# Kernel tuning notes

Hardware: AMD Instinct MI355X
Metric: run time of the kernel (lower is better)

Reference implementation:

```python
import jax, jax.numpy as jnp
import numpy as np

MARGIN = 0.2
W_HARD = 1.0
W_SOFT = 0.0
NORMALIZE = True
PD_EPS = 1e-6  # torch F.pairwise_distance eps used inside TripletMarginLoss


def setup_inputs() -> dict:
    key = jax.random.key(0)
    k1, k2, k3 = jax.random.split(key, 3)
    N, D = 8192, 128
    z = jax.random.normal(k1, (N, D), dtype=jnp.float32)
    labels = jax.random.randint(k2, (N,), 0, 16, dtype=jnp.int32)
    subjects = jax.random.randint(k3, (N,), 0, 32, dtype=jnp.int32)
    return {"z": z, "labels": labels, "subjects": subjects}


def _batch_hard(z, pos_mask, neg_mask, margin):
    # pairwise euclidean distances (cdist p=2); mining indices are ints, so
    # stop_gradient keeps vjp clean (matches torch: argmax/argmin detach).
    sq = jnp.sum(z * z, axis=1)
    d2 = sq[:, None] + sq[None, :] - 2.0 * (z @ z.T)
    dist = jax.lax.stop_gradient(jnp.sqrt(jnp.maximum(d2, 0.0)))
    inf = jnp.asarray(jnp.inf, dist.dtype)
    p_idx = jnp.argmax(jnp.where(pos_mask, dist, -inf), axis=1)  # hardest positive
    n_idx = jnp.argmin(jnp.where(neg_mask, dist, inf), axis=1)   # hardest negative
    valid = jnp.any(pos_mask, axis=1) & jnp.any(neg_mask, axis=1)
    a, p, n = z, z[p_idx], z[n_idx]
    d_ap = jnp.sqrt(jnp.sum((a - p + PD_EPS) ** 2, axis=1))
    d_an = jnp.sqrt(jnp.sum((a - n + PD_EPS) ** 2, axis=1))
    per = jnp.maximum(d_ap - d_an + margin, 0.0)
    cnt = jnp.sum(valid)
    loss = jnp.sum(per * valid) / jnp.maximum(cnt, 1).astype(per.dtype)
    return jnp.where(cnt > 0, loss, 0.0)


def reference(z, labels, subjects):
    if NORMALIZE:
        z = z / jnp.maximum(jnp.linalg.norm(z, axis=1, keepdims=True), 1e-12)
    N = z.shape[0]
    same_class = labels[:, None] == labels[None, :]
    same_subj = subjects[:, None] == subjects[None, :]
    not_eye = ~jnp.eye(N, dtype=bool)
    loss = 0.0
    denom = 0.0
    if W_HARD != 0:
        pos_hard = same_class & ~same_subj & not_eye
        neg_hard = ~same_class & same_subj & not_eye
        loss = loss + W_HARD * _batch_hard(z, pos_hard, neg_hard, MARGIN)
        denom += abs(W_HARD)
    if W_SOFT != 0:
        pos_soft = same_class & same_subj & not_eye
        neg_soft = ~same_class & ~same_subj & not_eye
        loss = loss + W_SOFT * _batch_hard(z, pos_soft, neg_soft, MARGIN)
        denom += abs(W_SOFT)
    return loss / max(denom, 1e-12)
```

## Files before the change

kernel.cpp:

```cpp
#include <hip/hip_runtime.h>
#include <math.h>

#define N 8192
#define D 128
#define MARGIN 0.2f
#define PD_EPS 1e-6f
#define NCHUNK 16
#define CHUNKJ (N / NCHUNK)

typedef __attribute__((ext_vector_type(8))) short bf16x8;
typedef __attribute__((ext_vector_type(4))) float f32x4;

__device__ __forceinline__ unsigned short f2bf(float f) {
    unsigned u = __float_as_uint(f);
    u += 0x7FFFu + ((u >> 16) & 1u);
    return (unsigned short)(u >> 16);
}
__device__ __forceinline__ unsigned umn(unsigned a, unsigned b) { return a < b ? a : b; }
__device__ __forceinline__ unsigned umx(unsigned a, unsigned b) { return a > b ? a : b; }

__global__ __launch_bounds__(256) void k_normalize(const float* __restrict__ z,
                                                   const int* __restrict__ labels,
                                                   const int* __restrict__ subjects,
                                                   unsigned short* __restrict__ znb,
                                                   float* __restrict__ invn,
                                                   int* __restrict__ meta) {
    int row  = blockIdx.x * 4 + (threadIdx.x >> 6);
    int lane = threadIdx.x & 63;
    float2 v = ((const float2*)(z + (size_t)row * D))[lane];
    float ss = v.x * v.x + v.y * v.y;
    #pragma unroll
    for (int m = 1; m < 64; m <<= 1) ss += __shfl_xor(ss, m, 64);
    float norm = fmaxf(sqrtf(ss), 1e-12f);
    float ox = v.x / norm, oy = v.y / norm;
    ushort2 b; b.x = f2bf(ox); b.y = f2bf(oy);
    ((ushort2*)(znb + (size_t)row * D))[lane] = b;
    if (lane == 0) {
        invn[row] = 1.0f / norm;
        meta[row] = labels[row] * 32 + subjects[row];
    }
}

__global__ __launch_bounds__(256, 2) void k_mine(const unsigned short* __restrict__ znb,
                                                 const int* __restrict__ meta,
                                                 unsigned* __restrict__ posk,
                                                 unsigned* __restrict__ negk) {
    const int wave = threadIdx.x >> 6;
    const int lane = threadIdx.x & 63;
    const int m    = lane & 15;
    const int quad = lane >> 4;
    const int iw   = (blockIdx.x * 4 + wave) * 64;
    const int jc   = blockIdx.y;
    const int jbase = jc * CHUNKJ;

    bf16x8 afrag[4][4];
    #pragma unroll
    for (int u = 0; u < 4; ++u)
        #pragma unroll
        for (int s = 0; s < 4; ++s)
            afrag[u][s] = *(const bf16x8*)(znb + (size_t)(iw + u * 16 + m) * D + s * 32 + quad * 8);

    int mi[16];
    #pragma unroll
    for (int u = 0; u < 4; ++u)
        #pragma unroll
        for (int r = 0; r < 4; ++r)
            mi[u * 4 + r] = meta[iw + u * 16 + quad * 4 + r];

    unsigned bp[16], bn[16];
    #pragma unroll
    for (int s = 0; s < 16; ++s) { bp[s] = 0xFFFFFFFFu; bn[s] = 0u; }

    for (int t = 0; t < CHUNKJ / 64; ++t) {
        const int jt = jbase + t * 64;

        f32x4 acc[4][4];
        #pragma unroll
        for (int u = 0; u < 4; ++u)
            #pragma unroll
            for (int v = 0; v < 4; ++v)
                acc[u][v] = (f32x4){0.f, 0.f, 0.f, 0.f};

        #pragma unroll
        for (int s = 0; s < 4; ++s) {
            bf16x8 bf[4];
            #pragma unroll
            for (int v = 0; v < 4; ++v)
                bf[v] = *(const bf16x8*)(znb + (size_t)(jt + v * 16 + m) * D + s * 32 + quad * 8);
            #pragma unroll
            for (int u = 0; u < 4; ++u)
                #pragma unroll
                for (int v = 0; v < 4; ++v)
                    acc[u][v] = __builtin_amdgcn_mfma_f32_16x16x32_bf16(afrag[u][s], bf[v], acc[u][v], 0, 0, 0);
        }

        #pragma unroll
        for (int v = 0; v < 4; ++v) {
            const int jv  = jt + v * 16 + m;
            const int mjv = meta[jv];
            #pragma unroll
            for (int u = 0; u < 4; ++u)
                #pragma unroll
                for (int r = 0; r < 4; ++r) {
                    float dot = acc[u][v][r];
                    unsigned key = (__float_as_uint(dot + 2.0f) & 0xFFFFE000u) | (unsigned)jv;
                    int x = mi[u * 4 + r] ^ mjv;
                    bool pos = (x != 0) && (x < 32);
                    bool neg = (x != 0) && ((x & 31) == 0);
                    bp[u * 4 + r] = umn(bp[u * 4 + r], pos ? key : 0xFFFFFFFFu);
                    bn[u * 4 + r] = umx(bn[u * 4 + r], neg ? key : 0u);
                }
        }
    }

    #pragma unroll
    for (int mm = 1; mm < 16; mm <<= 1)
        #pragma unroll
        for (int s = 0; s < 16; ++s) {
            bp[s] = umn(bp[s], (unsigned)__shfl_xor((int)bp[s], mm, 64));
            bn[s] = umx(bn[s], (unsigned)__shfl_xor((int)bn[s], mm, 64));
        }
    if (m == 0) {
        #pragma unroll
        for (int u = 0; u < 4; ++u)
            #pragma unroll
            for (int r = 0; r < 4; ++r) {
                int i = iw + u * 16 + quad * 4 + r;
                posk[(size_t)jc * N + i] = bp[u * 4 + r];
                negk[(size_t)jc * N + i] = bn[u * 4 + r];
            }
    }
}

__global__ __launch_bounds__(256) void k_final(const float* __restrict__ z,
                                               const float* __restrict__ invn,
                                               const unsigned* __restrict__ posk,
                                               const unsigned* __restrict__ negk,
                                               float* __restrict__ per, float* __restrict__ vld) {
    int row  = blockIdx.x * 4 + (threadIdx.x >> 6);
    int lane = threadIdx.x & 63;
    unsigned mp = 0xFFFFFFFFu, mn = 0u;
    #pragma unroll
    for (int c = 0; c < NCHUNK; ++c) {
        mp = umn(mp, posk[(size_t)c * N + row]);
        mn = umx(mn, negk[(size_t)c * N + row]);
    }
    bool valid = (mp != 0xFFFFFFFFu) && (mn != 0u);
    int pi = valid ? (int)(mp & 8191u) : 0;
    int ni = valid ? (int)(mn & 8191u) : 0;
    float ia = invn[row], ip = invn[pi], iq = invn[ni];
    float2 a = ((const float2*)(z + (size_t)row * D))[lane];
    float2 p = ((const float2*)(z + (size_t)pi  * D))[lane];
    float2 q = ((const float2*)(z + (size_t)ni  * D))[lane];
    float dx = a.x * ia - p.x * ip + PD_EPS, dy = a.y * ia - p.y * ip + PD_EPS;
    float sap = dx * dx + dy * dy;
    dx = a.x * ia - q.x * iq + PD_EPS; dy = a.y * ia - q.y * iq + PD_EPS;
    float san = dx * dx + dy * dy;
    #pragma unroll
    for (int m = 1; m < 64; m <<= 1) {
        sap += __shfl_xor(sap, m, 64);
        san += __shfl_xor(san, m, 64);
    }
    if (lane == 0) {
        float l = fmaxf(sqrtf(sap) - sqrtf(san) + MARGIN, 0.0f);
        per[row] = valid ? l : 0.0f;
        vld[row] = valid ? 1.0f : 0.0f;
    }
}

__global__ __launch_bounds__(256) void k_reduce(const float* __restrict__ per,
                                                const float* __restrict__ vld,
                                                float* __restrict__ out) {
    __shared__ float s1[256], s2[256];
    int t = threadIdx.x;
    float a = 0.f, b = 0.f;
    for (int i = t; i < N; i += 256) { a += per[i]; b += vld[i]; }
    s1[t] = a; s2[t] = b;
    __syncthreads();
    for (int w = 128; w > 0; w >>= 1) {
        if (t < w) { s1[t] += s1[t + w]; s2[t] += s2[t + w]; }
        __syncthreads();
    }
    if (t == 0) {
        float cnt = s2[0];
        out[0] = (cnt > 0.f) ? s1[0] / fmaxf(cnt, 1.f) : 0.f;
    }
}

extern "C" void kernel_launch(void* const* d_in, const int* in_sizes, int n_in,
                              void* d_out, int out_size, void* d_ws, size_t ws_size,
                              hipStream_t stream) {
    const float* z        = (const float*)d_in[0];
    const int*   labels   = (const int*)d_in[1];
    const int*   subjects = (const int*)d_in[2];
    float* out = (float*)d_out;

    char* ws = (char*)d_ws;
    unsigned short* znb = (unsigned short*)(ws);
    float*    invn = (float*)   (ws + 2097152);
    int*      meta = (int*)     (ws + 2129920);
    unsigned* posk = (unsigned*)(ws + 2162688);
    unsigned* negk = (unsigned*)(ws + 2686976);
    float*    per  = (float*)   (ws + 3211264);
    float*    vld  = (float*)   (ws + 3244032);

    k_normalize<<<dim3(N / 4), dim3(256), 0, stream>>>(z, labels, subjects, znb, invn, meta);
    k_mine<<<dim3(32, NCHUNK), dim3(256), 0, stream>>>(znb, meta, posk, negk);
    k_final<<<dim3(N / 4), dim3(256), 0, stream>>>(z, invn, posk, negk, per, vld);
    k_reduce<<<dim3(1), dim3(256), 0, stream>>>(per, vld, out);
}
```

Baseline: 116.9 us.

## Double mining chunks, raise occupancy, hoist meta loads, fuse final reduce

The j-dimension split for the mining kernel goes from 16 to 32 chunks, which doubles the grid to 1024 blocks so the 256 CUs are better filled, and the occupancy hint on k_mine rises from 2 to 4 blocks per CU. The per-column meta loads are hoisted ahead of the MFMA loop so their latency overlaps the matrix math. The separate single-block reduce kernel is folded into k_final through a last-block-done atomic ticket, removing one launch. In exchange, k_final reads twice as many partial keys, the higher occupancy target may force register spills given the large fragment and accumulator arrays, and the ticket counter must be reset correctly on every call.

```diff
diff --git a/kernel.cpp b/kernel.cpp
--- a/kernel.cpp
+++ b/kernel.cpp
@@ -5,7 +5,7 @@
 #define D 128
 #define MARGIN 0.2f
 #define PD_EPS 1e-6f
-#define NCHUNK 16
+#define NCHUNK 32
 #define CHUNKJ (N / NCHUNK)
 
 typedef __attribute__((ext_vector_type(8))) short bf16x8;
@@ -24,7 +24,9 @@
                                                    const int* __restrict__ subjects,
                                                    unsigned short* __restrict__ znb,
                                                    float* __restrict__ invn,
-                                                   int* __restrict__ meta) {
+                                                   int* __restrict__ meta,
+                                                   unsigned* __restrict__ tick) {
+    if (blockIdx.x == 0 && threadIdx.x == 0) *tick = 0u;
     int row  = blockIdx.x * 4 + (threadIdx.x >> 6);
     int lane = threadIdx.x & 63;
     float2 v = ((const float2*)(z + (size_t)row * D))[lane];
@@ -41,7 +43,7 @@
     }
 }
 
-__global__ __launch_bounds__(256, 2) void k_mine(const unsigned short* __restrict__ znb,
+__global__ __launch_bounds__(256, 4) void k_mine(const unsigned short* __restrict__ znb,
                                                  const int* __restrict__ meta,
                                                  unsigned* __restrict__ posk,
                                                  unsigned* __restrict__ negk) {
@@ -74,6 +76,10 @@
     for (int t = 0; t < CHUNKJ / 64; ++t) {
         const int jt = jbase + t * 64;
 
+        int mjv[4];
+        #pragma unroll
+        for (int v = 0; v < 4; ++v) mjv[v] = meta[jt + v * 16 + m];
+
         f32x4 acc[4][4];
         #pragma unroll
         for (int u = 0; u < 4; ++u)
@@ -96,15 +102,14 @@
 
         #pragma unroll
         for (int v = 0; v < 4; ++v) {
-            const int jv  = jt + v * 16 + m;
-            const int mjv = meta[jv];
+            const int jv = jt + v * 16 + m;
             #pragma unroll
             for (int u = 0; u < 4; ++u)
                 #pragma unroll
                 for (int r = 0; r < 4; ++r) {
                     float dot = acc[u][v][r];
                     unsigned key = (__float_as_uint(dot + 2.0f) & 0xFFFFE000u) | (unsigned)jv;
-                    int x = mi[u * 4 + r] ^ mjv;
+                    int x = mi[u * 4 + r] ^ mjv[v];
                     bool pos = (x != 0) && (x < 32);
                     bool neg = (x != 0) && ((x & 31) == 0);
                     bp[u * 4 + r] = umn(bp[u * 4 + r], pos ? key : 0xFFFFFFFFu);
@@ -136,7 +141,11 @@
                                                const float* __restrict__ invn,
                                                const unsigned* __restrict__ posk,
                                                const unsigned* __restrict__ negk,
-                                               float* __restrict__ per, float* __restrict__ vld) {
+                                               float* __restrict__ per, float* __restrict__ vld,
+                                               unsigned* __restrict__ tick,
+                                               float* __restrict__ out) {
+    __shared__ float s1[256], s2[256];
+    __shared__ int lastFlag;
     int row  = blockIdx.x * 4 + (threadIdx.x >> 6);
     int lane = threadIdx.x & 63;
     unsigned mp = 0xFFFFFFFFu, mn = 0u;
@@ -166,24 +175,28 @@
         per[row] = valid ? l : 0.0f;
         vld[row] = valid ? 1.0f : 0.0f;
     }
-}
-
-__global__ __launch_bounds__(256) void k_reduce(const float* __restrict__ per,
-                                                const float* __restrict__ vld,
-                                                float* __restrict__ out) {
-    __shared__ float s1[256], s2[256];
-    int t = threadIdx.x;
-    float a = 0.f, b = 0.f;
-    for (int i = t; i < N; i += 256) { a += per[i]; b += vld[i]; }
-    s1[t] = a; s2[t] = b;
+
+    __threadfence();
     __syncthreads();
-    for (int w = 128; w > 0; w >>= 1) {
-        if (t < w) { s1[t] += s1[t + w]; s2[t] += s2[t + w]; }
+    if (threadIdx.x == 0)
+        lastFlag = (atomicAdd(tick, 1u) == gridDim.x - 1);
+    __syncthreads();
+    if (lastFlag) {
+        __threadfence();
+        int t = threadIdx.x;
+        float a2 = 0.f, b2 = 0.f;
+        for (int i = t; i < N; i += 256) { a2 += per[i]; b2 += vld[i]; }
+        s1[t] = a2; s2[t] = b2;
         __syncthreads();
-    }
-    if (t == 0) {
-        float cnt = s2[0];
-        out[0] = (cnt > 0.f) ? s1[0] / fmaxf(cnt, 1.f) : 0.f;
+        for (int w = 128; w > 0; w >>= 1) {
+            if (t < w) { s1[t] += s1[t + w]; s2[t] += s2[t + w]; }
+            __syncthreads();
+        }
+        if (t == 0) {
+            float cnt = s2[0];
+            out[0] = (cnt > 0.f) ? s1[0] / fmaxf(cnt, 1.f) : 0.f;
+            *tick = 0u;
+        }
     }
 }
 
@@ -200,12 +213,12 @@
     float*    invn = (float*)   (ws + 2097152);
     int*      meta = (int*)     (ws + 2129920);
     unsigned* posk = (unsigned*)(ws + 2162688);
-    unsigned* negk = (unsigned*)(ws + 2686976);
-    float*    per  = (float*)   (ws + 3211264);
-    float*    vld  = (float*)   (ws + 3244032);
-
-    k_normalize<<<dim3(N / 4), dim3(256), 0, stream>>>(z, labels, subjects, znb, invn, meta);
+    unsigned* negk = (unsigned*)(ws + 3211264);
+    float*    per  = (float*)   (ws + 4259840);
+    float*    vld  = (float*)   (ws + 4292608);
+    unsigned* tick = (unsigned*)(ws + 4325376);
+
+    k_normalize<<<dim3(N / 4), dim3(256), 0, stream>>>(z, labels, subjects, znb, invn, meta, tick);
     k_mine<<<dim3(32, NCHUNK), dim3(256), 0, stream>>>(znb, meta, posk, negk);
-    k_final<<<dim3(N / 4), dim3(256), 0, stream>>>(z, invn, posk, negk, per, vld);
-    k_reduce<<<dim3(1), dim3(256), 0, stream>>>(per, vld, out);
-}
+    k_final<<<dim3(N / 4), dim3(256), 0, stream>>>(z, invn, posk, negk, per, vld, tick, out);
+}
```

Measured after the change: 353.4 us. 202% more time.
